# Optimization experiments

Measured on AMD Instinct MI355X. Metric: run time of the kernel, lower is better.

The kernel has to match this reference:

```python
import jax, jax.numpy as jnp
import numpy as np

IN_OUT_CHANNELS = [192, 128, 32]  # in_channels + [out_channel]
HIST_BIN = IN_OUT_CHANNELS[0] // 3  # 64 bins per color channel


def _per_channel_hist(img, bins):
    """torch.histc(ch, bins, min=0, max=1) per (image, channel), vectorized.

    img: [N, 3, H, W] with values in [0, 1]. Returns [N, 3*bins] float32.
    """
    N, C, H, W = img.shape
    x = img.reshape(N * C, H * W)
    # bin index = floor(x * bins), last bin closed at 1.0
    idx = jnp.clip((x * bins).astype(jnp.int32), 0, bins - 1)
    offsets = jnp.arange(N * C, dtype=jnp.int32)[:, None] * bins
    flat = (idx + offsets).reshape(-1)
    hist = jnp.zeros((N * C * bins,), jnp.float32).at[flat].add(1.0)
    return hist.reshape(N, C * bins)


def setup_inputs() -> dict:
    key = jax.random.key(0)
    k1, k2 = jax.random.split(key)
    img = jax.random.uniform(k1, (16, 3, 1024, 1024), dtype=jnp.float32)
    total_params = sum(
        IN_OUT_CHANNELS[i] * IN_OUT_CHANNELS[i + 1] + IN_OUT_CHANNELS[i + 1]
        for i in range(len(IN_OUT_CHANNELS) - 1)
    ) + IN_OUT_CHANNELS[-1]
    # small scale so the dynamic-MLP logits stay in a sane range
    params = jax.random.normal(k2, (total_params,), dtype=jnp.float32) * 1e-3
    return {"img": img, "params": params}


def reference(img, params):
    N = img.shape[0]
    # histogram is detached in the original module
    hist_feat = jax.lax.stop_gradient(_per_channel_hist(img, HIST_BIN))
    par_idx = 0
    layers = len(IN_OUT_CHANNELS) - 1
    for idx in range(layers):
        in_ch = IN_OUT_CHANNELS[idx]
        out_ch = IN_OUT_CHANNELS[idx + 1]
        w = params[par_idx : par_idx + in_ch * out_ch].reshape(in_ch, out_ch)
        par_idx += in_ch * out_ch
        b = params[par_idx : par_idx + out_ch]
        par_idx += out_ch
        hist_feat = jnp.matmul(hist_feat, w) + b
        if idx != layers - 1:
            hist_feat = jax.nn.relu(hist_feat)
    # original: global_params = params[par_idx] (scalar), broadcast over (N, out)
    global_params = params[par_idx]
    out_params = jax.nn.sigmoid(global_params + hist_feat)
    return out_params
```

## Files before the change

### kernel.cpp

```cpp
#include <hip/hip_runtime.h>
#include <math.h>

#define N_IMG       16
#define N_CH        3
#define PLANES      (N_IMG * N_CH)
#define BINS        64
#define PLANE_ELEMS (1024 * 1024)
#define PLANE_VEC   (PLANE_ELEMS / 4)
#define BLOCKS_PER_PLANE 32
#define HIST_THREADS 256
#define PER_BLOCK   (PLANE_VEC / BLOCKS_PER_PLANE)

#define C0 192
#define C1 128
#define C2 32
#define OFF_W0 0
#define OFF_B0 (C0 * C1)
#define OFF_W1 (OFF_B0 + C1)
#define OFF_B1 (OFF_W1 + C1 * C2)
#define OFF_G  (OFF_B1 + C2)

typedef float fx4 __attribute__((ext_vector_type(4)));

__global__ __launch_bounds__(HIST_THREADS) void hist_kernel(
    const fx4* __restrict__ img, unsigned int* __restrict__ partial)
{
    __shared__ unsigned int h[BINS * 64];

    const int tid  = threadIdx.x;
    const int lane = tid & 63;

    for (int i = tid; i < BINS * 64; i += HIST_THREADS) h[i] = 0u;
    __syncthreads();

    const int plane = blockIdx.y;
    const fx4* p = img + (size_t)plane * PLANE_VEC
                       + (size_t)blockIdx.x * PER_BLOCK + tid;

    #pragma unroll 2
    for (int it = 0; it < PER_BLOCK / (HIST_THREADS * 4); ++it) {
        fx4 a = __builtin_nontemporal_load(&p[0]);
        fx4 b = __builtin_nontemporal_load(&p[HIST_THREADS]);
        fx4 c = __builtin_nontemporal_load(&p[2 * HIST_THREADS]);
        fx4 d = __builtin_nontemporal_load(&p[3 * HIST_THREADS]);
        p += 4 * HIST_THREADS;

        #define PROC(v)                                                 \
        {                                                               \
            int e0 = __float2int_rz((v).x * 64.0f);                     \
            int e1 = __float2int_rz((v).y * 64.0f);                     \
            int e2 = __float2int_rz((v).z * 64.0f);                     \
            int e3 = __float2int_rz((v).w * 64.0f);                     \
            atomicAdd(&h[(e0 << 6) + lane], 1u);                        \
            atomicAdd(&h[(e1 << 6) + lane], 1u);                        \
            atomicAdd(&h[(e2 << 6) + lane], 1u);                        \
            atomicAdd(&h[(e3 << 6) + lane], 1u);                        \
        }
        PROC(a) PROC(b) PROC(c) PROC(d)
        #undef PROC
    }
    __syncthreads();

    if (tid < BINS) {
        unsigned int s = 0;
        #pragma unroll
        for (int l = 0; l < 64; ++l) s += h[(tid << 6) + l];
        partial[(size_t)(plane * BINS + tid) * BLOCKS_PER_PLANE + blockIdx.x] = s;
    }
}

__global__ __launch_bounds__(512) void mlp_kernel(
    const unsigned int* __restrict__ partial,
    const float* __restrict__ params,
    float* __restrict__ out)
{
    __shared__ float feat[N_IMG * C0];
    __shared__ float h1[N_IMG * C1];

    const int tid = threadIdx.x;

    for (int i = tid; i < PLANES * BINS; i += 512) {
        const uint4* q = (const uint4*)(partial + (size_t)i * BLOCKS_PER_PLANE);
        unsigned int s = 0;
        #pragma unroll
        for (int v = 0; v < BLOCKS_PER_PLANE / 4; ++v) {
            uint4 u = q[v];
            s += u.x + u.y + u.z + u.w;
        }
        feat[i] = (float)s;
    }
    __syncthreads();

    const float* W0 = params + OFF_W0;
    const float* b0 = params + OFF_B0;
    const float* W1 = params + OFF_W1;
    const float* b1 = params + OFF_B1;
    const float  g  = params[OFF_G];

    for (int t = tid; t < N_IMG * C1; t += 512) {
        const int n = t >> 7, j = t & 127;
        float acc = b0[j];
        const float* f = feat + n * C0;
        #pragma unroll 8
        for (int i = 0; i < C0; ++i)
            acc = fmaf(f[i], W0[i * C1 + j], acc);
        h1[t] = fmaxf(acc, 0.0f);
    }
    __syncthreads();

    {
        const int n = tid >> 5, k = tid & 31;
        float acc = b1[k];
        const float* hh = h1 + n * C1;
        #pragma unroll 8
        for (int j = 0; j < C1; ++j)
            acc = fmaf(hh[j], W1[j * C2 + k], acc);
        float x = g + acc;
        out[tid] = 1.0f / (1.0f + expf(-x));
    }
}

extern "C" void kernel_launch(void* const* d_in, const int* in_sizes, int n_in,
                              void* d_out, int out_size, void* d_ws, size_t ws_size,
                              hipStream_t stream)
{
    const float* img    = (const float*)d_in[0];
    const float* params = (const float*)d_in[1];
    float* out          = (float*)d_out;
    unsigned int* partial = (unsigned int*)d_ws;

    dim3 grid(BLOCKS_PER_PLANE, PLANES);
    hist_kernel<<<grid, HIST_THREADS, 0, stream>>>((const fx4*)img, partial);
    mlp_kernel<<<1, 512, 0, stream>>>(partial, params, out);
}
```

Baseline: 293.9 us.

## Fuse histogram and MLP into one kernel with last-block ticket

Merges the histogram and MLP kernels into a single launch. Each block atomically adds its per-bin counts into a global feature buffer, and the last block to take a ticket runs the MLP and then resets the buffer and ticket. This removes one kernel launch and the partial-sum reduction pass, at the cost of global atomics and a serial MLP tail that runs on a single 256-thread block. Smem bin reads are also rotated per thread to avoid bank conflicts.

```diff
diff --git a/kernel.cpp b/kernel.cpp
--- a/kernel.cpp
+++ b/kernel.cpp
@@ -10,6 +10,7 @@
 #define BLOCKS_PER_PLANE 32
 #define HIST_THREADS 256
 #define PER_BLOCK   (PLANE_VEC / BLOCKS_PER_PLANE)
+#define TOTAL_BLOCKS (PLANES * BLOCKS_PER_PLANE)
 
 #define C0 192
 #define C1 128
@@ -22,10 +23,16 @@
 
 typedef float fx4 __attribute__((ext_vector_type(4)));
 
-__global__ __launch_bounds__(HIST_THREADS) void hist_kernel(
-    const fx4* __restrict__ img, unsigned int* __restrict__ partial)
+__device__ unsigned int g_feat[PLANES * BINS];
+__device__ unsigned int g_ticket;
+
+__global__ __launch_bounds__(HIST_THREADS) void fused_kernel(
+    const fx4* __restrict__ img,
+    const float* __restrict__ params,
+    float* __restrict__ out)
 {
-    __shared__ unsigned int h[BINS * 64];
+    __shared__ unsigned int smem[5120];
+    unsigned int* h = smem;
 
     const int tid  = threadIdx.x;
     const int lane = tid & 63;
@@ -64,30 +71,30 @@
     if (tid < BINS) {
         unsigned int s = 0;
         #pragma unroll
-        for (int l = 0; l < 64; ++l) s += h[(tid << 6) + l];
-        partial[(size_t)(plane * BINS + tid) * BLOCKS_PER_PLANE + blockIdx.x] = s;
+        for (int l = 0; l < 64; ++l)
+            s += h[(tid << 6) + ((tid + l) & 63)];
+        atomicAdd(&g_feat[plane * BINS + tid], s);
     }
-}
 
-__global__ __launch_bounds__(512) void mlp_kernel(
-    const unsigned int* __restrict__ partial,
-    const float* __restrict__ params,
-    float* __restrict__ out)
-{
-    __shared__ float feat[N_IMG * C0];
-    __shared__ float h1[N_IMG * C1];
+    __syncthreads();
+    __shared__ unsigned int s_last;
+    if (tid == 0) {
+        __threadfence();
+        unsigned int t = atomicAdd(&g_ticket, 1u);
+        s_last = (t == TOTAL_BLOCKS - 1) ? 1u : 0u;
+    }
+    __syncthreads();
+    if (!s_last) return;
 
-    const int tid = threadIdx.x;
+    __threadfence();
 
-    for (int i = tid; i < PLANES * BINS; i += 512) {
-        const uint4* q = (const uint4*)(partial + (size_t)i * BLOCKS_PER_PLANE);
-        unsigned int s = 0;
-        #pragma unroll
-        for (int v = 0; v < BLOCKS_PER_PLANE / 4; ++v) {
-            uint4 u = q[v];
-            s += u.x + u.y + u.z + u.w;
-        }
-        feat[i] = (float)s;
+    float* feat = (float*)smem;
+    float* h1   = (float*)(smem + 3072);
+
+    {
+        volatile const unsigned int* gf = g_feat;
+        for (int i = tid; i < PLANES * BINS; i += HIST_THREADS)
+            feat[i] = (float)gf[i];
     }
     __syncthreads();
 
@@ -97,7 +104,7 @@
     const float* b1 = params + OFF_B1;
     const float  g  = params[OFF_G];
 
-    for (int t = tid; t < N_IMG * C1; t += 512) {
+    for (int t = tid; t < N_IMG * C1; t += HIST_THREADS) {
         const int n = t >> 7, j = t & 127;
         float acc = b0[j];
         const float* f = feat + n * C0;
@@ -108,15 +115,26 @@
     }
     __syncthreads();
 
-    {
-        const int n = tid >> 5, k = tid & 31;
+    for (int t = tid; t < N_IMG * C2; t += HIST_THREADS) {
+        const int n = t >> 5, k = t & 31;
         float acc = b1[k];
         const float* hh = h1 + n * C1;
         #pragma unroll 8
         for (int j = 0; j < C1; ++j)
             acc = fmaf(hh[j], W1[j * C2 + k], acc);
         float x = g + acc;
-        out[tid] = 1.0f / (1.0f + expf(-x));
+        out[t] = 1.0f / (1.0f + expf(-x));
+    }
+    __syncthreads();
+
+    {
+        volatile unsigned int* gf = g_feat;
+        for (int i = tid; i < PLANES * BINS; i += HIST_THREADS)
+            gf[i] = 0u;
+        if (tid == 0) {
+            __threadfence();
+            *(volatile unsigned int*)&g_ticket = 0u;
+        }
     }
 }
 
@@ -127,9 +145,8 @@
     const float* img    = (const float*)d_in[0];
     const float* params = (const float*)d_in[1];
     float* out          = (float*)d_out;
-    unsigned int* partial = (unsigned int*)d_ws;
+    (void)d_ws; (void)ws_size;
 
     dim3 grid(BLOCKS_PER_PLANE, PLANES);
-    hist_kernel<<<grid, HIST_THREADS, 0, stream>>>((const fx4*)img, partial);
-    mlp_kernel<<<1, 512, 0, stream>>>(partial, params, out);
+    fused_kernel<<<grid, HIST_THREADS, 0, stream>>>((const fx4*)img, params, out);
 }
```

After: 375.4 us. 27.7% more time.

## Split MLP across one block per image and compact partial histograms to u16

Applied to the files above, without the earlier changes.

The MLP kernel now runs one 128-thread block per image instead of a single 512-thread block, so the small matmuls are spread over 16 CUs. Partial histogram counts are stored as 16-bit values in a block-major layout, which makes the reduction reads coalesced and shrinks workspace traffic. The final per-bin reduction in the histogram kernel uses a rotated lane index to avoid LDS bank conflicts. The 16-bit counts rely on each block's per-bin count staying below 65536, which holds here because each block handles 32768 elements.

```diff
diff --git a/kernel.cpp b/kernel.cpp
--- a/kernel.cpp
+++ b/kernel.cpp
@@ -10,6 +10,7 @@
 #define BLOCKS_PER_PLANE 32
 #define HIST_THREADS 256
 #define PER_BLOCK   (PLANE_VEC / BLOCKS_PER_PLANE)
+#define FEATS       (PLANES * BINS)
 
 #define C0 192
 #define C1 128
@@ -23,7 +24,7 @@
 typedef float fx4 __attribute__((ext_vector_type(4)));
 
 __global__ __launch_bounds__(HIST_THREADS) void hist_kernel(
-    const fx4* __restrict__ img, unsigned int* __restrict__ partial)
+    const fx4* __restrict__ img, unsigned short* __restrict__ partial)
 {
     __shared__ unsigned int h[BINS * 64];
 
@@ -64,30 +65,30 @@
     if (tid < BINS) {
         unsigned int s = 0;
         #pragma unroll
-        for (int l = 0; l < 64; ++l) s += h[(tid << 6) + l];
-        partial[(size_t)(plane * BINS + tid) * BLOCKS_PER_PLANE + blockIdx.x] = s;
+        for (int l = 0; l < 64; ++l)
+            s += h[(tid << 6) + ((tid + l) & 63)];
+        partial[(size_t)blockIdx.x * FEATS + plane * BINS + tid] =
+            (unsigned short)s;
     }
 }
 
-__global__ __launch_bounds__(512) void mlp_kernel(
-    const unsigned int* __restrict__ partial,
+__global__ __launch_bounds__(128) void mlp_kernel(
+    const unsigned short* __restrict__ partial,
     const float* __restrict__ params,
     float* __restrict__ out)
 {
-    __shared__ float feat[N_IMG * C0];
-    __shared__ float h1[N_IMG * C1];
+    __shared__ float feat[C0];
+    __shared__ float h1[C1];
 
+    const int n   = blockIdx.x;
     const int tid = threadIdx.x;
 
-    for (int i = tid; i < PLANES * BINS; i += 512) {
-        const uint4* q = (const uint4*)(partial + (size_t)i * BLOCKS_PER_PLANE);
+    for (int f = tid; f < C0; f += 128) {
         unsigned int s = 0;
         #pragma unroll
-        for (int v = 0; v < BLOCKS_PER_PLANE / 4; ++v) {
-            uint4 u = q[v];
-            s += u.x + u.y + u.z + u.w;
-        }
-        feat[i] = (float)s;
+        for (int pb = 0; pb < BLOCKS_PER_PLANE; ++pb)
+            s += partial[(size_t)pb * FEATS + n * C0 + f];
+        feat[f] = (float)s;
     }
     __syncthreads();
 
@@ -97,26 +98,24 @@
     const float* b1 = params + OFF_B1;
     const float  g  = params[OFF_G];
 
-    for (int t = tid; t < N_IMG * C1; t += 512) {
-        const int n = t >> 7, j = t & 127;
+    {
+        const int j = tid;
         float acc = b0[j];
-        const float* f = feat + n * C0;
         #pragma unroll 8
         for (int i = 0; i < C0; ++i)
-            acc = fmaf(f[i], W0[i * C1 + j], acc);
-        h1[t] = fmaxf(acc, 0.0f);
+            acc = fmaf(feat[i], W0[i * C1 + j], acc);
+        h1[j] = fmaxf(acc, 0.0f);
     }
     __syncthreads();
 
-    {
-        const int n = tid >> 5, k = tid & 31;
+    if (tid < C2) {
+        const int k = tid;
         float acc = b1[k];
-        const float* hh = h1 + n * C1;
         #pragma unroll 8
         for (int j = 0; j < C1; ++j)
-            acc = fmaf(hh[j], W1[j * C2 + k], acc);
+            acc = fmaf(h1[j], W1[j * C2 + k], acc);
         float x = g + acc;
-        out[tid] = 1.0f / (1.0f + expf(-x));
+        out[n * C2 + k] = 1.0f / (1.0f + expf(-x));
     }
 }
 
@@ -127,9 +126,9 @@
     const float* img    = (const float*)d_in[0];
     const float* params = (const float*)d_in[1];
     float* out          = (float*)d_out;
-    unsigned int* partial = (unsigned int*)d_ws;
+    unsigned short* partial = (unsigned short*)d_ws;
 
     dim3 grid(BLOCKS_PER_PLANE, PLANES);
     hist_kernel<<<grid, HIST_THREADS, 0, stream>>>((const fx4*)img, partial);
-    mlp_kernel<<<1, 512, 0, stream>>>(partial, params, out);
+    mlp_kernel<<<N_IMG, 128, 0, stream>>>(partial, params, out);
 }
```

After: 278.8 us. -5.1%, faster.
